# Performance work log

Measured on AMD Instinct MI355X. Metric: run time of the kernel, lower is better.

Reference implementation:

```python
import jax, jax.numpy as jnp
import numpy as np


def setup_inputs() -> dict:
    key = jax.random.key(0)
    ks = jax.random.split(key, 6)
    B, Din, Dout, K, L = 4096, 4096, 4096, 256, 4
    # scale params like kaiming-ish init to keep activations O(1)
    hin = jax.random.normal(ks[0], (B, Din), dtype=jnp.float32)
    S1s = jax.random.normal(ks[1], (L, Din, K), dtype=jnp.float32) / np.sqrt(Din)
    S2s = jax.random.normal(ks[2], (L, K, Dout), dtype=jnp.float32) / np.sqrt(K)
    U1s = jax.random.normal(ks[3], (L, K, Dout), dtype=jnp.float32) / np.sqrt(K)
    U2s = jax.random.normal(ks[4], (L, Din, K), dtype=jnp.float32) / np.sqrt(Din)
    bias = jax.random.normal(ks[5], (Dout,), dtype=jnp.float32)
    return {"hin": hin, "S1s": S1s, "S2s": S2s, "U1s": U1s, "U2s": U2s, "bias": bias}


def reference(hin, S1s, S2s, U1s, U2s, bias):
    # out = (sum_l (hin @ S1s_l @ U1s_l + hin @ U2s_l @ S2s_l) + bias) / (2 L)
    L = S1s.shape[0]
    a = jnp.einsum('bd,ldk->lbk', hin, S1s)      # [L, B, K]
    t1 = jnp.einsum('lbk,lko->bo', a, U1s)       # [B, Dout]
    b = jnp.einsum('bd,ldk->lbk', hin, U2s)      # [L, B, K]
    t2 = jnp.einsum('lbk,lko->bo', b, S2s)       # [B, Dout]
    return (t1 + t2 + bias) / (2.0 * L)
```

## Files before the change

kernel.cpp:

```cpp
#include <hip/hip_runtime.h>
#include <stdint.h>

typedef unsigned short u16;
typedef __bf16 bf16x8 __attribute__((ext_vector_type(8)));
typedef float f32x4 __attribute__((ext_vector_type(4)));

#define DIN 4096
#define DOUT 4096
#define BB 4096
#define KR 256
#define RK 2048

__device__ __forceinline__ u16 f2bf(float f) {
    union { float f; unsigned u; } v; v.f = f;
    unsigned r = v.u + 0x7FFFu + ((v.u >> 16) & 1u);
    return (u16)(r >> 16);
}

__device__ __forceinline__ void gl_lds16(const void* g, void* l) {
    __builtin_amdgcn_global_load_lds((const __attribute__((address_space(1))) void*)g,
                                     (__attribute__((address_space(3))) void*)l,
                                     16, 0, 0);
}

__global__ __launch_bounds__(256) void cvt_f32_bf16(const float* __restrict__ src,
                                                    u16* __restrict__ dst, int n8) {
    int i = blockIdx.x * blockDim.x + threadIdx.x;
    if (i >= n8) return;
    const float4* s = reinterpret_cast<const float4*>(src) + (size_t)i * 2;
    float4 a = s[0], b = s[1];
    uint4 o;
    o.x = f2bf(a.x) | ((unsigned)f2bf(a.y) << 16);
    o.y = f2bf(a.z) | ((unsigned)f2bf(a.w) << 16);
    o.z = f2bf(b.x) | ((unsigned)f2bf(b.y) << 16);
    o.w = f2bf(b.z) | ((unsigned)f2bf(b.w) << 16);
    reinterpret_cast<uint4*>(dst)[i] = o;
}

__global__ __launch_bounds__(256) void pack_w1t(const float* __restrict__ S1s,
                                                const float* __restrict__ U2s,
                                                u16* __restrict__ W1T) {
    __shared__ u16 lds[64][68];
    int b  = blockIdx.x;
    int bd = b & 63;
    int bk = (b >> 6) & 3;
    int lb = b >> 8;
    int l = lb >> 1, br = lb & 1;
    const float* src = (br ? U2s : S1s) + (size_t)l * DIN * KR;
    int t = threadIdx.x;
    int d0 = bd * 64, k0 = bk * 64;
    int r0 = l * 512 + br * 256 + k0;
    #pragma unroll
    for (int p = 0; p < 4; ++p) {
        int dl = p * 16 + (t >> 4);
        int kc = (t & 15) * 4;
        float4 v = *reinterpret_cast<const float4*>(src + (size_t)(d0 + dl) * KR + k0 + kc);
        ushort4 pk;
        pk.x = f2bf(v.x); pk.y = f2bf(v.y); pk.z = f2bf(v.z); pk.w = f2bf(v.w);
        *reinterpret_cast<ushort4*>(&lds[dl][kc]) = pk;
    }
    __syncthreads();
    #pragma unroll
    for (int p = 0; p < 2; ++p) {
        int kl = p * 32 + (t >> 3);
        int d8 = t & 7;
        u16 tmp[8];
        #pragma unroll
        for (int j = 0; j < 8; ++j) tmp[j] = lds[d8 * 8 + j][kl];
        uint4 o;
        o.x = tmp[0] | ((unsigned)tmp[1] << 16);
        o.y = tmp[2] | ((unsigned)tmp[3] << 16);
        o.z = tmp[4] | ((unsigned)tmp[5] << 16);
        o.w = tmp[6] | ((unsigned)tmp[7] << 16);
        *reinterpret_cast<uint4*>(W1T + (size_t)(r0 + kl) * DIN + d0 + d8 * 8) = o;
    }
}

__global__ __launch_bounds__(256) void pack_w2t(const float* __restrict__ U1s,
                                                const float* __restrict__ S2s,
                                                u16* __restrict__ W2T) {
    __shared__ u16 lds[64][68];
    int b  = blockIdx.x;
    int bo = b & 63;
    int bk = (b >> 6) & 3;
    int lb = b >> 8;
    int l = lb >> 1, br = lb & 1;
    const float* src = (br ? S2s : U1s) + (size_t)l * KR * DOUT;
    int t = threadIdx.x;
    int o0 = bo * 64, k0 = bk * 64;
    #pragma unroll
    for (int p = 0; p < 4; ++p) {
        int kl = p * 16 + (t >> 4);
        int ol = (t & 15) * 4;
        float4 v = *reinterpret_cast<const float4*>(src + (size_t)(k0 + kl) * DOUT + o0 + ol);
        ushort4 pk;
        pk.x = f2bf(v.x); pk.y = f2bf(v.y); pk.z = f2bf(v.z); pk.w = f2bf(v.w);
        *reinterpret_cast<ushort4*>(&lds[kl][ol]) = pk;
    }
    __syncthreads();
    #pragma unroll
    for (int p = 0; p < 2; ++p) {
        int ol = p * 32 + (t >> 3);
        int k8 = t & 7;
        u16 tmp[8];
        #pragma unroll
        for (int j = 0; j < 8; ++j) tmp[j] = lds[k8 * 8 + j][ol];
        uint4 o;
        o.x = tmp[0] | ((unsigned)tmp[1] << 16);
        o.y = tmp[2] | ((unsigned)tmp[3] << 16);
        o.z = tmp[4] | ((unsigned)tmp[5] << 16);
        o.w = tmp[6] | ((unsigned)tmp[7] << 16);
        *reinterpret_cast<uint4*>(W2T + (size_t)(o0 + ol) * RK + l * 512 + br * 256 + k0 + k8 * 8) = o;
    }
}

template <int BN, int MW, int EPI>
__global__ __launch_bounds__(512) void gemm8(const u16* __restrict__ A,
                                             const u16* __restrict__ Bt,
                                             void* __restrict__ Cv,
                                             const float* __restrict__ bias,
                                             int N, int Kd) {
    extern __shared__ char smem[];
    constexpr int BHB = (BN == 256) ? 16384 : 8192;
    constexpr int BROWS = BN / 2;
    constexpr int NW = 8 / MW;
    constexpr int MF = 128 / (16 * MW);
    constexpr int MROW = 128 / MW;
    char* ldsA = smem;
    char* ldsB = smem + 65536;

    const int tid = threadIdx.x;
    const int l = tid & 63;
    const int wv = tid >> 6;
    const int wr = wv / NW;
    const int wc = wv % NW;

    int bid = blockIdx.x;
    bid = (bid & 7) * 32 + (bid >> 3);
    const int mt = bid >> 4, nt = bid & 15;
    const int m0 = mt * 256, n0 = nt * BN;

    const int NITER = Kd >> 7;

    size_t aoff[2], boff[2];
    {
        #pragma unroll
        for (int r = 0; r < 2; ++r) {
            int lin = (r * 512 + tid) * 16;
            int s = lin ^ (((lin >> 7) & 7) << 4);
            int e = s >> 1;
            size_t o = (size_t)(e >> 6) * Kd + (e & 63);
            aoff[r] = (size_t)m0 * Kd + o;
            boff[r] = (size_t)n0 * Kd + o;
        }
    }

    auto issueA = [&](int h, int b, size_t kb) {
        char* d = ldsA + (((b << 1) | h) * 16384) + tid * 16;
        gl_lds16(A + aoff[0] + (size_t)h * 128 * Kd + kb, d);
        gl_lds16(A + aoff[1] + (size_t)h * 128 * Kd + kb, d + 8192);
    };
    auto issueB = [&](int h, int b, size_t kb) {
        char* d = ldsB + (((b << 1) | h) * BHB) + tid * 16;
        gl_lds16(Bt + boff[0] + (size_t)h * BROWS * Kd + kb, d);
        if constexpr (BN == 256)
            gl_lds16(Bt + boff[1] + (size_t)h * BROWS * Kd + kb, d + 8192);
    };

    int rowAb[MF];
    #pragma unroll
    for (int m = 0; m < MF; ++m) rowAb[m] = (wr * MROW + m * 16 + (l & 15)) * 128;
    int rowBb[2];
    #pragma unroll
    for (int n = 0; n < 2; ++n) rowBb[n] = (wc * 32 + n * 16 + (l & 15)) * 128;
    const int cc0 = ((l >> 4) ^ (l & 7)) << 4;

    f32x4 acc[2][2][MF][2] = {};
    bf16x8 af[MF][2];
    bf16x8 bf[2][2][2];

#define PHASE(BUF, MH, NH, RDA, RDB, ISSUE_STMT, VM) do {                         \
    ISSUE_STMT;                                                                   \
    const char* Ah_ = ldsA + (((BUF) << 1) | (MH)) * 16384;                       \
    const char* Bh_ = ldsB + (((BUF) << 1) | (NH)) * BHB;                         \
    if (RDA) { _Pragma("unroll") for (int m_ = 0; m_ < MF; ++m_) {                \
        af[m_][0] = *(const bf16x8*)(Ah_ + (rowAb[m_] | cc0));                    \
        af[m_][1] = *(const bf16x8*)(Ah_ + ((rowAb[m_] | cc0) ^ 64)); } }         \
    if (RDB) { _Pragma("unroll") for (int n_ = 0; n_ < 2; ++n_) {                 \
        bf[NH][n_][0] = *(const bf16x8*)(Bh_ + (rowBb[n_] | cc0));                \
        bf[NH][n_][1] = *(const bf16x8*)(Bh_ + ((rowBb[n_] | cc0) ^ 64)); } }     \
    __builtin_amdgcn_s_setprio(1);                                                \
    _Pragma("unroll") for (int m_ = 0; m_ < MF; ++m_)                             \
        _Pragma("unroll") for (int n_ = 0; n_ < 2; ++n_) {                        \
            acc[MH][NH][m_][n_] = __builtin_amdgcn_mfma_f32_16x16x32_bf16(        \
                af[m_][0], bf[NH][n_][0], acc[MH][NH][m_][n_], 0, 0, 0);          \
            acc[MH][NH][m_][n_] = __builtin_amdgcn_mfma_f32_16x16x32_bf16(        \
                af[m_][1], bf[NH][n_][1], acc[MH][NH][m_][n_], 0, 0, 0); }        \
    __builtin_amdgcn_s_setprio(0);                                                \
    if (VM) { if (BN == 256) asm volatile("s_waitcnt vmcnt(4)" ::: "memory");     \
              else           asm volatile("s_waitcnt vmcnt(3)" ::: "memory"); }   \
    asm volatile("" ::: "memory");                                                \
    __builtin_amdgcn_s_barrier();                                                 \
} while (0)

    issueA(0, 0, 0);  issueB(0, 0, 0);
    issueA(1, 0, 0);  issueB(1, 0, 0);
    issueA(0, 1, 64); issueB(0, 1, 64);
    if (BN == 256) asm volatile("s_waitcnt vmcnt(4)" ::: "memory");
    else           asm volatile("s_waitcnt vmcnt(3)" ::: "memory");
    __builtin_amdgcn_s_barrier();

    for (int J = 0; J < NITER; ++J) {
        const size_t kc = (size_t)J << 7;
        PHASE(0, 0, 0, 1, 1, issueA(1, 1, kc + 64),  0);
        PHASE(0, 0, 1, 0, 1, issueB(1, 1, kc + 64),  0);
        PHASE(0, 1, 1, 1, 0, issueA(0, 0, kc + 128), 0);
        PHASE(0, 1, 0, 0, 0, issueB(0, 0, kc + 128), 1);
        PHASE(1, 0, 0, 1, 1, issueA(1, 0, kc + 128), 0);
        PHASE(1, 0, 1, 0, 1, issueB(1, 0, kc + 128), 0);
        PHASE(1, 1, 1, 1, 0, issueA(0, 1, kc + 192), 0);
        PHASE(1, 1, 0, 0, 0, issueB(0, 1, kc + 192), 1);
    }
#undef PHASE

    const int colc = l & 15, rb = (l >> 4) * 4;
    #pragma unroll
    for (int mh = 0; mh < 2; ++mh)
    #pragma unroll
    for (int nh = 0; nh < 2; ++nh)
    #pragma unroll
    for (int m = 0; m < MF; ++m)
    #pragma unroll
    for (int n = 0; n < 2; ++n) {
        int c = n0 + nh * (BN / 2) + wc * 32 + n * 16 + colc;
        int r0r = m0 + mh * 128 + wr * MROW + m * 16 + rb;
        if (EPI == 0) {
            u16* Cb = (u16*)Cv;
            #pragma unroll
            for (int j = 0; j < 4; ++j)
                Cb[(size_t)(r0r + j) * N + c] = f2bf(acc[mh][nh][m][n][j]);
        } else {
            float* Cf = (float*)Cv;
            float bv = bias[c];
            #pragma unroll
            for (int j = 0; j < 4; ++j)
                Cf[(size_t)(r0r + j) * N + c] = (acc[mh][nh][m][n][j] + bv) * 0.125f;
        }
    }
}

extern "C" void kernel_launch(void* const* d_in, const int* in_sizes, int n_in,
                              void* d_out, int out_size, void* d_ws, size_t ws_size,
                              hipStream_t stream) {
    const float* hin  = (const float*)d_in[0];
    const float* S1s  = (const float*)d_in[1];
    const float* S2s  = (const float*)d_in[2];
    const float* U1s  = (const float*)d_in[3];
    const float* U2s  = (const float*)d_in[4];
    const float* bias = (const float*)d_in[5];
    float* out = (float*)d_out;

    const size_t SZ_HIN = (size_t)BB * DIN * 2 + 512;
    const size_t SZ_W   = (size_t)RK * DIN * 2 + 512;
    const size_t SZ_A   = (size_t)BB * RK * 2 + 512;
    if (ws_size < SZ_HIN + SZ_W + SZ_A) return;
    u16* hinbf = (u16*)d_ws;
    u16* Wx    = (u16*)((char*)d_ws + SZ_HIN);
    u16* abf   = (u16*)((char*)d_ws + SZ_HIN + SZ_W);

    (void)hipFuncSetAttribute(reinterpret_cast<const void*>(&gemm8<128, 4, 0>),
                              hipFuncAttributeMaxDynamicSharedMemorySize, 98304);
    (void)hipFuncSetAttribute(reinterpret_cast<const void*>(&gemm8<256, 2, 1>),
                              hipFuncAttributeMaxDynamicSharedMemorySize, 131072);

    pack_w1t<<<64 * 4 * 8, 256, 0, stream>>>(S1s, U2s, Wx);
    cvt_f32_bf16<<<(BB * DIN / 8) / 256, 256, 0, stream>>>(hin, hinbf, BB * DIN / 8);
    gemm8<128, 4, 0><<<256, 512, 98304, stream>>>(hinbf, Wx, abf, nullptr, RK, DIN);
    pack_w2t<<<64 * 4 * 8, 256, 0, stream>>>(U1s, S2s, Wx);
    gemm8<256, 2, 1><<<256, 512, 131072, stream>>>(abf, Wx, out, bias, DOUT, RK);
}
```

Baseline: 166.1 us.

## Software-pipeline LDS fragment reads one phase ahead with double-buffered registers

Restructures the GEMM main loop so the LDS fragment reads for the next MFMA phase are issued before the current phase's MFMAs, using two A-fragment sets and two B-fragment sets. Scheduling barriers keep those reads ahead of the MFMAs. The global-to-LDS prefetch also goes deeper, with the prologue issuing all eight half-tiles and vmcnt thresholds doubled. The goal is to hide LDS read latency and global load latency behind matrix math. The cost is extra VGPR pressure, which may reduce occupancy or cause spills, and correctness now depends on the more delicate waitcnt and barrier ordering.

```diff
diff --git a/kernel.cpp b/kernel.cpp
--- a/kernel.cpp
+++ b/kernel.cpp
@@ -176,52 +176,58 @@
     const int cc0 = ((l >> 4) ^ (l & 7)) << 4;
 
     f32x4 acc[2][2][MF][2] = {};
-    bf16x8 af[MF][2];
-    bf16x8 bf[2][2][2];
-
-#define PHASE(BUF, MH, NH, RDA, RDB, ISSUE_STMT, VM) do {                         \
-    ISSUE_STMT;                                                                   \
-    const char* Ah_ = ldsA + (((BUF) << 1) | (MH)) * 16384;                       \
-    const char* Bh_ = ldsB + (((BUF) << 1) | (NH)) * BHB;                         \
-    if (RDA) { _Pragma("unroll") for (int m_ = 0; m_ < MF; ++m_) {                \
-        af[m_][0] = *(const bf16x8*)(Ah_ + (rowAb[m_] | cc0));                    \
-        af[m_][1] = *(const bf16x8*)(Ah_ + ((rowAb[m_] | cc0) ^ 64)); } }         \
-    if (RDB) { _Pragma("unroll") for (int n_ = 0; n_ < 2; ++n_) {                 \
-        bf[NH][n_][0] = *(const bf16x8*)(Bh_ + (rowBb[n_] | cc0));                \
-        bf[NH][n_][1] = *(const bf16x8*)(Bh_ + ((rowBb[n_] | cc0) ^ 64)); } }     \
-    __builtin_amdgcn_s_setprio(1);                                                \
-    _Pragma("unroll") for (int m_ = 0; m_ < MF; ++m_)                             \
-        _Pragma("unroll") for (int n_ = 0; n_ < 2; ++n_) {                        \
-            acc[MH][NH][m_][n_] = __builtin_amdgcn_mfma_f32_16x16x32_bf16(        \
-                af[m_][0], bf[NH][n_][0], acc[MH][NH][m_][n_], 0, 0, 0);          \
-            acc[MH][NH][m_][n_] = __builtin_amdgcn_mfma_f32_16x16x32_bf16(        \
-                af[m_][1], bf[NH][n_][1], acc[MH][NH][m_][n_], 0, 0, 0); }        \
-    __builtin_amdgcn_s_setprio(0);                                                \
-    if (VM) { if (BN == 256) asm volatile("s_waitcnt vmcnt(4)" ::: "memory");     \
-              else           asm volatile("s_waitcnt vmcnt(3)" ::: "memory"); }   \
-    asm volatile("" ::: "memory");                                                \
-    __builtin_amdgcn_s_barrier();                                                 \
-} while (0)
-
-    issueA(0, 0, 0);  issueB(0, 0, 0);
-    issueA(1, 0, 0);  issueB(1, 0, 0);
-    issueA(0, 1, 64); issueB(0, 1, 64);
-    if (BN == 256) asm volatile("s_waitcnt vmcnt(4)" ::: "memory");
-    else           asm volatile("s_waitcnt vmcnt(3)" ::: "memory");
+    bf16x8 afA[MF][2], afB[MF][2];
+    bf16x8 bf0[2][2], bf1[2][2];
+
+#define RDA(SET, B_, H_) do { const char* Ah_ = ldsA + (((B_) << 1) | (H_)) * 16384;  \
+    _Pragma("unroll") for (int m_ = 0; m_ < MF; ++m_) {                               \
+        SET[m_][0] = *(const bf16x8*)(Ah_ + (rowAb[m_] | cc0));                       \
+        SET[m_][1] = *(const bf16x8*)(Ah_ + ((rowAb[m_] | cc0) ^ 64)); } } while (0)
+#define RDB(DST, B_, H_) do { const char* Bh_ = ldsB + (((B_) << 1) | (H_)) * BHB;    \
+    _Pragma("unroll") for (int n_ = 0; n_ < 2; ++n_) {                                \
+        DST[n_][0] = *(const bf16x8*)(Bh_ + (rowBb[n_] | cc0));                       \
+        DST[n_][1] = *(const bf16x8*)(Bh_ + ((rowBb[n_] | cc0) ^ 64)); } } while (0)
+#define MM(MH, NH, ASET, BREG) do {                                                   \
+    __builtin_amdgcn_s_setprio(1);                                                    \
+    _Pragma("unroll") for (int m_ = 0; m_ < MF; ++m_)                                 \
+        _Pragma("unroll") for (int n_ = 0; n_ < 2; ++n_) {                            \
+            acc[MH][NH][m_][n_] = __builtin_amdgcn_mfma_f32_16x16x32_bf16(            \
+                ASET[m_][0], BREG[n_][0], acc[MH][NH][m_][n_], 0, 0, 0);              \
+            acc[MH][NH][m_][n_] = __builtin_amdgcn_mfma_f32_16x16x32_bf16(            \
+                ASET[m_][1], BREG[n_][1], acc[MH][NH][m_][n_], 0, 0, 0); }            \
+    __builtin_amdgcn_s_setprio(0); } while (0)
+#define SB0 __builtin_amdgcn_sched_barrier(0)
+#define VMW do { if constexpr (BN == 256)                                             \
+                     asm volatile("s_waitcnt vmcnt(8)" ::: "memory");                 \
+                 else asm volatile("s_waitcnt vmcnt(6)" ::: "memory"); } while (0)
+#define ENDP do { asm volatile("" ::: "memory");                                      \
+                  __builtin_amdgcn_s_barrier(); } while (0)
+
+    issueA(0, 0, 0);  issueB(0, 0, 0);  issueB(1, 0, 0);  issueA(1, 0, 0);
+    issueA(0, 1, 64); issueB(0, 1, 64); issueB(1, 1, 64); issueA(1, 1, 64);
+    VMW;
     __builtin_amdgcn_s_barrier();
+    RDA(afA, 0, 0);
+    RDB(bf0, 0, 0);
 
     for (int J = 0; J < NITER; ++J) {
-        const size_t kc = (size_t)J << 7;
-        PHASE(0, 0, 0, 1, 1, issueA(1, 1, kc + 64),  0);
-        PHASE(0, 0, 1, 0, 1, issueB(1, 1, kc + 64),  0);
-        PHASE(0, 1, 1, 1, 0, issueA(0, 0, kc + 128), 0);
-        PHASE(0, 1, 0, 0, 0, issueB(0, 0, kc + 128), 1);
-        PHASE(1, 0, 0, 1, 1, issueA(1, 0, kc + 128), 0);
-        PHASE(1, 0, 1, 0, 1, issueB(1, 0, kc + 128), 0);
-        PHASE(1, 1, 1, 1, 0, issueA(0, 1, kc + 192), 0);
-        PHASE(1, 1, 0, 0, 0, issueB(0, 1, kc + 192), 1);
-    }
-#undef PHASE
+        const size_t kb0 = ((size_t)J << 7) + 128;
+        const size_t kb1 = kb0 + 64;
+        issueA(0, 0, kb0); RDB(bf1, 0, 1); SB0; MM(0, 0, afA, bf0); ENDP;
+        issueB(0, 0, kb0); RDA(afB, 0, 1); SB0; MM(0, 1, afA, bf1); VMW; ENDP;
+        issueB(1, 0, kb0); RDA(afA, 1, 0); SB0; MM(1, 1, afB, bf1); ENDP;
+        issueA(1, 0, kb0); MM(1, 0, afB, bf0); RDB(bf0, 1, 0); VMW; ENDP;
+        issueA(0, 1, kb1); RDB(bf1, 1, 1); SB0; MM(0, 0, afA, bf0); ENDP;
+        issueB(0, 1, kb1); RDA(afB, 1, 1); SB0; MM(0, 1, afA, bf1); VMW; ENDP;
+        issueB(1, 1, kb1); RDA(afA, 0, 0); SB0; MM(1, 1, afB, bf1); ENDP;
+        issueA(1, 1, kb1); MM(1, 0, afB, bf0); RDB(bf0, 0, 0); VMW; ENDP;
+    }
+#undef RDA
+#undef RDB
+#undef MM
+#undef SB0
+#undef VMW
+#undef ENDP
 
     const int colc = l & 15, rb = (l >> 4) * 4;
     #pragma unroll
```

Measured after the change: 221.0 us. 33.0% more time.
